# Kernel optimization log

Measured on AMD Instinct MI355X. Metric: run time of the kernel, lower is better.

## Reference

```python
import jax, jax.numpy as jnp
import numpy as np

B, L, HID = 16, 512, 768
HEADS, M = 12, 4
EMB, BLK, NER, NCLS = 768, 8, 6, 97


def setup_inputs() -> dict:
    key = jax.random.key(0)
    ks = jax.random.split(key, 10)
    return {
        "sequence_output": jax.random.normal(ks[0], (B, L, HID), jnp.float32),
        "attention": jax.random.uniform(ks[1], (B, HEADS, L, L), jnp.float32),
        "entity_pos": jax.random.randint(ks[2], (B, 2, M), 0, L - 2),
        "hs_ner_tags": jax.random.uniform(ks[3], (B, NER), jnp.float32),
        "ts_ner_tags": jax.random.uniform(ks[4], (B, NER), jnp.float32),
        "Wh": jax.random.normal(ks[5], (EMB, 2 * HID + NER), jnp.float32) * 0.02,
        "bh": jnp.zeros((EMB,), jnp.float32),
        "Wt": jax.random.normal(ks[6], (EMB, 2 * HID + NER), jnp.float32) * 0.02,
        "bt": jnp.zeros((EMB,), jnp.float32),
        "Wb": jax.random.normal(ks[7], (NCLS, EMB * BLK), jnp.float32) * 0.02,
        "bb": jnp.zeros((NCLS,), jnp.float32),
    }


def reference(sequence_output, attention, entity_pos, hs_ner_tags, ts_ner_tags,
              Wh, bh, Wt, bt, Wb, bb):
    b_idx = jnp.arange(B)[:, None, None]            # [B,1,1]
    starts = entity_pos + 1                         # [B,2,M] (all < L by construction)

    # entity embeddings: gather mention token embeddings, logsumexp-pool over mentions
    ment_emb = sequence_output[b_idx, starts]       # [B,2,M,HID]
    ent_emb = jax.scipy.special.logsumexp(ment_emb, axis=2)  # [B,2,HID]

    # entity attentions: gather mention attention rows, mean-pool over mentions
    attn_t = attention.transpose(0, 2, 1, 3)        # [B,L,HEADS,L]
    ment_att = attn_t[b_idx, starts]                # [B,2,M,HEADS,L]
    ent_att = ment_att.mean(axis=2)                 # [B,2,HEADS,L]

    hs, ts = ent_emb[:, 0], ent_emb[:, 1]           # [B,HID]
    h_att, t_att = ent_att[:, 0], ent_att[:, 1]     # [B,HEADS,L]

    ht_att = (h_att * t_att).mean(axis=1)           # [B,L]
    ht_att = ht_att / (ht_att.sum(axis=1, keepdims=True) + 1e-5)
    rs = jnp.einsum('bld,bl->bd', sequence_output, ht_att)  # [B,HID]

    hs2 = jnp.tanh(jnp.concatenate([hs, rs, hs_ner_tags], axis=1) @ Wh.T + bh)
    ts2 = jnp.tanh(jnp.concatenate([ts, rs, ts_ner_tags], axis=1) @ Wt.T + bt)

    b1 = hs2.reshape(B, EMB // BLK, BLK)
    b2 = ts2.reshape(B, EMB // BLK, BLK)
    bl = (b1[:, :, :, None] * b2[:, :, None, :]).reshape(B, EMB * BLK)
    logits = bl @ Wb.T + bb                         # [B, NCLS]
    return logits
```

## Files before the change

kernel.cpp:

```cpp
#include <hip/hip_runtime.h>
#include <math.h>

#define B 16
#define L 512
#define HID 768
#define HEADS 12
#define M 4
#define EMB 768
#define BLK 8
#define NER 6
#define NCLS 97
#define CAT (2*HID + NER)
#define EB (EMB*BLK)
#define NCH 8

__global__ void k_att(const float* __restrict__ att, const float* __restrict__ seq,
                      const int* __restrict__ epos,
                      float* __restrict__ pp, float* __restrict__ ent,
                      float* __restrict__ rs) {
    int b = blockIdx.x, h = blockIdx.y;
    __shared__ int ss[2][M];
    if (threadIdx.x < 2*M) {
        int e = threadIdx.x >> 2, m = threadIdx.x & 3;
        ss[e][m] = epos[(b*2+e)*M + m] + 1;
    }
    __syncthreads();

    int l = threadIdx.x;
    const float* ah = att + ((size_t)b*HEADS + h)*L*L;
    float a0 = 0.f, a1 = 0.f;
    #pragma unroll
    for (int m = 0; m < M; ++m) {
        a0 += ah[(size_t)ss[0][m]*L + l];
        a1 += ah[(size_t)ss[1][m]*L + l];
    }
    pp[((size_t)b*HEADS + h)*L + l] = a0*a1;

    if (h < 2) {
        const float* base = seq + (size_t)b*L*HID;
        for (int d = threadIdx.x; d < HID; d += 512) {
            float v0 = base[(size_t)ss[h][0]*HID + d];
            float v1 = base[(size_t)ss[h][1]*HID + d];
            float v2 = base[(size_t)ss[h][2]*HID + d];
            float v3 = base[(size_t)ss[h][3]*HID + d];
            float mx = fmaxf(fmaxf(v0, v1), fmaxf(v2, v3));
            float s = expf(v0-mx) + expf(v1-mx) + expf(v2-mx) + expf(v3-mx);
            ent[((size_t)h*B + b)*HID + d] = mx + logf(s);
        }
    } else if (h == 2) {
        for (int d = threadIdx.x; d < HID; d += 512) rs[b*HID + d] = 0.f;
    }
}

__launch_bounds__(192)
__global__ void k_rs(const float* __restrict__ seq, const float* __restrict__ pp,
                     float* __restrict__ rs) {
    int b = blockIdx.x, ch = blockIdx.y;
    __shared__ float sraw[L];
    __shared__ float red[3];
    __shared__ float sinv;
    float psum = 0.f;
    for (int l = threadIdx.x; l < L; l += 192) {
        float r = 0.f;
        #pragma unroll
        for (int h = 0; h < HEADS; ++h) r += pp[((size_t)b*HEADS + h)*L + l];
        r *= (1.f/(M*M*HEADS));
        sraw[l] = r;
        psum += r;
    }
    for (int off = 32; off; off >>= 1) psum += __shfl_down(psum, off);
    int wid = threadIdx.x >> 6, lane = threadIdx.x & 63;
    if (lane == 0) red[wid] = psum;
    __syncthreads();
    if (threadIdx.x == 0) sinv = 1.f/(red[0] + red[1] + red[2] + 1e-5f);
    __syncthreads();
    float inv = sinv;

    const float4* sp = (const float4*)(seq + (size_t)b*L*HID + (size_t)ch*(L/NCH)*HID);
    float4 acc = make_float4(0.f, 0.f, 0.f, 0.f);
    for (int i = 0; i < L/NCH; ++i) {
        float w = sraw[ch*(L/NCH) + i] * inv;
        float4 v = sp[i*(HID/4) + threadIdx.x];
        acc.x += v.x*w; acc.y += v.y*w; acc.z += v.z*w; acc.w += v.w*w;
    }
    float* rp = rs + b*HID + threadIdx.x*4;
    atomicAdd(rp+0, acc.x);
    atomicAdd(rp+1, acc.y);
    atomicAdd(rp+2, acc.z);
    atomicAdd(rp+3, acc.w);
}

__launch_bounds__(512)
__global__ void k_proj(const float* __restrict__ Wh, const float* __restrict__ bh,
                       const float* __restrict__ Wt, const float* __restrict__ bt,
                       const float* __restrict__ ent, const float* __restrict__ rs,
                       const float* __restrict__ hner, const float* __restrict__ tner,
                       float* __restrict__ out) {
    int t = blockIdx.y, zh = blockIdx.z;
    __shared__ float actA[CAT*4];
    __shared__ float actB[CAT*4];
    const float* e0  = ent + (size_t)t*B*HID;
    const float* ner = t ? tner : hner;
    for (int idx = threadIdx.x; idx < CAT*8; idx += 512) {
        int k = idx >> 3, bi = idx & 7;
        int gb = zh*8 + bi;
        float v;
        if (k < HID)            v = e0[gb*HID + k];
        else if (k < 2*HID)     v = rs[gb*HID + (k - HID)];
        else                    v = ner[gb*NER + (k - 2*HID)];
        if (bi < 4) actA[k*4 + bi] = v; else actB[k*4 + bi - 4] = v;
    }
    __syncthreads();

    int wid = threadIdx.x >> 6, lane = threadIdx.x & 63;
    int j = blockIdx.x*8 + wid;
    const float* wrow = (t ? Wt : Wh) + (size_t)j*CAT;
    float acc[8];
    #pragma unroll
    for (int b = 0; b < 8; ++b) acc[b] = 0.f;
    for (int i = 0; i < 25; ++i) {
        int k = i*64 + lane;
        if (k < CAT) {
            float w = wrow[k];
            float4 a = *(const float4*)&actA[k*4];
            float4 c = *(const float4*)&actB[k*4];
            acc[0] += w*a.x; acc[1] += w*a.y; acc[2] += w*a.z; acc[3] += w*a.w;
            acc[4] += w*c.x; acc[5] += w*c.y; acc[6] += w*c.z; acc[7] += w*c.w;
        }
    }
    for (int off = 32; off; off >>= 1)
        #pragma unroll
        for (int b = 0; b < 8; ++b) acc[b] += __shfl_down(acc[b], off);
    if (lane == 0) {
        float bj = (t ? bt : bh)[j];
        #pragma unroll
        for (int b = 0; b < 8; ++b)
            out[((size_t)t*B + zh*8 + b)*EMB + j] = tanhf(acc[b] + bj);
    }
}

__global__ void k_bl(const float* __restrict__ proj, float* __restrict__ bl) {
    int b = blockIdx.x;
    const float* ph = proj + (size_t)b*EMB;
    const float* pt = proj + (size_t)B*EMB + (size_t)b*EMB;
    for (int i4 = threadIdx.x; i4 < EB/4; i4 += 512) {
        int k = i4*4;
        int g = k >> 6, r = (k >> 3) & 7, c0 = k & 7;
        float pr = ph[g*8 + r];
        float4 q = *(const float4*)(pt + g*8 + c0);
        float4 o = make_float4(pr*q.x, pr*q.y, pr*q.z, pr*q.w);
        ((float4*)(bl + (size_t)b*EB))[i4] = o;
    }
}

__launch_bounds__(512)
__global__ void k_logits(const float* __restrict__ Wb, const float* __restrict__ bb,
                         const float* __restrict__ bl, float* __restrict__ out) {
    int c = blockIdx.x;
    const float4* wr = (const float4*)(Wb + (size_t)c*EB);
    float acc[B];
    #pragma unroll
    for (int b = 0; b < B; ++b) acc[b] = 0.f;
    for (int i = threadIdx.x; i < EB/4; i += 512) {
        float4 w = wr[i];
        #pragma unroll
        for (int b = 0; b < B; ++b) {
            float4 v = ((const float4*)(bl + (size_t)b*EB))[i];
            acc[b] += w.x*v.x + w.y*v.y + w.z*v.z + w.w*v.w;
        }
    }
    int wid = threadIdx.x >> 6, lane = threadIdx.x & 63;
    for (int off = 32; off; off >>= 1)
        #pragma unroll
        for (int b = 0; b < B; ++b) acc[b] += __shfl_down(acc[b], off);
    __shared__ float partl[8][B];
    if (lane == 0)
        #pragma unroll
        for (int b = 0; b < B; ++b) partl[wid][b] = acc[b];
    __syncthreads();
    if (threadIdx.x < B) {
        int b = threadIdx.x;
        float s = 0.f;
        #pragma unroll
        for (int w = 0; w < 8; ++w) s += partl[w][b];
        out[b*NCLS + c] = s + bb[c];
    }
}

extern "C" void kernel_launch(void* const* d_in, const int* in_sizes, int n_in,
                              void* d_out, int out_size, void* d_ws, size_t ws_size,
                              hipStream_t stream) {
    const float* seq  = (const float*)d_in[0];
    const float* att  = (const float*)d_in[1];
    const int*   epos = (const int*)  d_in[2];
    const float* hner = (const float*)d_in[3];
    const float* tner = (const float*)d_in[4];
    const float* Wh   = (const float*)d_in[5];
    const float* bh   = (const float*)d_in[6];
    const float* Wt   = (const float*)d_in[7];
    const float* bt   = (const float*)d_in[8];
    const float* Wb   = (const float*)d_in[9];
    const float* bb   = (const float*)d_in[10];
    float* out = (float*)d_out;

    float* ws   = (float*)d_ws;
    float* pp   = ws;
    float* ent  = pp   + (size_t)B*HEADS*L;
    float* rs   = ent  + 2*B*HID;
    float* proj = rs   + B*HID;
    float* bl   = proj + 2*B*EMB;

    k_att   <<<dim3(B, HEADS), 512, 0, stream>>>(att, seq, epos, pp, ent, rs);
    k_rs    <<<dim3(B, NCH),   192, 0, stream>>>(seq, pp, rs);
    k_proj  <<<dim3(EMB/8, 2, 2), 512, 0, stream>>>(Wh, bh, Wt, bt, ent, rs, hner, tner, proj);
    k_bl    <<<dim3(B),        512, 0, stream>>>(proj, bl);
    k_logits<<<dim3(NCLS),     512, 0, stream>>>(Wb, bb, bl, out);
}
```

Baseline: 295.7 us.

## Precompute per-head normalizer sums in k_att and split rs/bl work across more blocks

k_att now reduces each head's product row to a partial sum Zp, so k_rs no longer sums all L weights per block and only computes the weights for its own chunk. k_rs chunk count goes from 8 to 16 and its inner loop is unrolled, which doubles the number of rs blocks. k_bl gets a second grid dimension so each thread writes a single float4. The extra block reduction in k_att adds a sync, and doubling the rs chunks doubles the atomicAdds.

```diff
diff --git a/kernel.cpp b/kernel.cpp
--- a/kernel.cpp
+++ b/kernel.cpp
@@ -12,12 +12,14 @@
 #define NCLS 97
 #define CAT (2*HID + NER)
 #define EB (EMB*BLK)
-#define NCH 8
+#define NCH 16
+#define LC (L/NCH)
+#define ISCALE (1.f/(M*M*HEADS))
 
 __global__ void k_att(const float* __restrict__ att, const float* __restrict__ seq,
                       const int* __restrict__ epos,
-                      float* __restrict__ pp, float* __restrict__ ent,
-                      float* __restrict__ rs) {
+                      float* __restrict__ pp, float* __restrict__ Zp,
+                      float* __restrict__ ent, float* __restrict__ rs) {
     int b = blockIdx.x, h = blockIdx.y;
     __shared__ int ss[2][M];
     if (threadIdx.x < 2*M) {
@@ -34,7 +36,21 @@
         a0 += ah[(size_t)ss[0][m]*L + l];
         a1 += ah[(size_t)ss[1][m]*L + l];
     }
-    pp[((size_t)b*HEADS + h)*L + l] = a0*a1;
+    float v = a0*a1;
+    pp[((size_t)b*HEADS + h)*L + l] = v;
+
+    float r = v;
+    for (int off = 32; off; off >>= 1) r += __shfl_down(r, off);
+    __shared__ float wsum[8];
+    int wid = threadIdx.x >> 6, lane = threadIdx.x & 63;
+    if (lane == 0) wsum[wid] = r;
+    __syncthreads();
+    if (threadIdx.x == 0) {
+        float t = 0.f;
+        #pragma unroll
+        for (int i = 0; i < 8; ++i) t += wsum[i];
+        Zp[b*HEADS + h] = t;
+    }
 
     if (h < 2) {
         const float* base = seq + (size_t)b*L*HID;
@@ -54,32 +70,27 @@
 
 __launch_bounds__(192)
 __global__ void k_rs(const float* __restrict__ seq, const float* __restrict__ pp,
-                     float* __restrict__ rs) {
+                     const float* __restrict__ Zp, float* __restrict__ rs) {
     int b = blockIdx.x, ch = blockIdx.y;
-    __shared__ float sraw[L];
-    __shared__ float red[3];
-    __shared__ float sinv;
-    float psum = 0.f;
-    for (int l = threadIdx.x; l < L; l += 192) {
+    __shared__ float sw[LC];
+    if (threadIdx.x < LC) {
+        float Z = 0.f;
+        #pragma unroll
+        for (int h = 0; h < HEADS; ++h) Z += Zp[b*HEADS + h];
+        float inv = ISCALE / (Z*ISCALE + 1e-5f);
+        int l = ch*LC + threadIdx.x;
         float r = 0.f;
         #pragma unroll
         for (int h = 0; h < HEADS; ++h) r += pp[((size_t)b*HEADS + h)*L + l];
-        r *= (1.f/(M*M*HEADS));
-        sraw[l] = r;
-        psum += r;
-    }
-    for (int off = 32; off; off >>= 1) psum += __shfl_down(psum, off);
-    int wid = threadIdx.x >> 6, lane = threadIdx.x & 63;
-    if (lane == 0) red[wid] = psum;
-    __syncthreads();
-    if (threadIdx.x == 0) sinv = 1.f/(red[0] + red[1] + red[2] + 1e-5f);
-    __syncthreads();
-    float inv = sinv;
-
-    const float4* sp = (const float4*)(seq + (size_t)b*L*HID + (size_t)ch*(L/NCH)*HID);
+        sw[threadIdx.x] = r * inv;
+    }
+    __syncthreads();
+
+    const float4* sp = (const float4*)(seq + (size_t)b*L*HID + (size_t)ch*LC*HID);
     float4 acc = make_float4(0.f, 0.f, 0.f, 0.f);
-    for (int i = 0; i < L/NCH; ++i) {
-        float w = sraw[ch*(L/NCH) + i] * inv;
+    #pragma unroll 8
+    for (int i = 0; i < LC; ++i) {
+        float w = sw[i];
         float4 v = sp[i*(HID/4) + threadIdx.x];
         acc.x += v.x*w; acc.y += v.y*w; acc.z += v.z*w; acc.w += v.w*w;
     }
@@ -141,16 +152,14 @@
 
 __global__ void k_bl(const float* __restrict__ proj, float* __restrict__ bl) {
     int b = blockIdx.x;
+    int i4 = blockIdx.y*512 + threadIdx.x;
     const float* ph = proj + (size_t)b*EMB;
     const float* pt = proj + (size_t)B*EMB + (size_t)b*EMB;
-    for (int i4 = threadIdx.x; i4 < EB/4; i4 += 512) {
-        int k = i4*4;
-        int g = k >> 6, r = (k >> 3) & 7, c0 = k & 7;
-        float pr = ph[g*8 + r];
-        float4 q = *(const float4*)(pt + g*8 + c0);
-        float4 o = make_float4(pr*q.x, pr*q.y, pr*q.z, pr*q.w);
-        ((float4*)(bl + (size_t)b*EB))[i4] = o;
-    }
+    int k = i4*4;
+    int g = k >> 6, r = (k >> 3) & 7, c0 = k & 7;
+    float pr = ph[g*8 + r];
+    float4 q = *(const float4*)(pt + g*8 + c0);
+    ((float4*)(bl + (size_t)b*EB))[i4] = make_float4(pr*q.x, pr*q.y, pr*q.z, pr*q.w);
 }
 
 __launch_bounds__(512)
@@ -205,14 +214,15 @@
 
     float* ws   = (float*)d_ws;
     float* pp   = ws;
-    float* ent  = pp   + (size_t)B*HEADS*L;
+    float* Zp   = pp   + (size_t)B*HEADS*L;
+    float* ent  = Zp   + B*HEADS;
     float* rs   = ent  + 2*B*HID;
     float* proj = rs   + B*HID;
     float* bl   = proj + 2*B*EMB;
 
-    k_att   <<<dim3(B, HEADS), 512, 0, stream>>>(att, seq, epos, pp, ent, rs);
-    k_rs    <<<dim3(B, NCH),   192, 0, stream>>>(seq, pp, rs);
+    k_att   <<<dim3(B, HEADS),    512, 0, stream>>>(att, seq, epos, pp, Zp, ent, rs);
+    k_rs    <<<dim3(B, NCH),      192, 0, stream>>>(seq, pp, Zp, rs);
     k_proj  <<<dim3(EMB/8, 2, 2), 512, 0, stream>>>(Wh, bh, Wt, bt, ent, rs, hner, tner, proj);
-    k_bl    <<<dim3(B),        512, 0, stream>>>(proj, bl);
-    k_logits<<<dim3(NCLS),     512, 0, stream>>>(Wb, bb, bl, out);
-}
+    k_bl    <<<dim3(B, 3),        512, 0, stream>>>(proj, bl);
+    k_logits<<<dim3(NCLS),        512, 0, stream>>>(Wb, bb, bl, out);
+}
```

Result: no change. 297.3 us (+0.5%).
